# Performance work log

Measured on AMD Instinct MI355X. Metric: run time of the kernel, lower is better.

## Reference

```python
import jax, jax.numpy as jnp
import numpy as np

NUM_BINS = 16
TAU = 0.05
EPS_SUM = 1e-8
EPS_LOG = 1e-10


def _entropy(counts):
    # counts: (dim, bins) -> (dim,) entropy in bits
    probs = counts / jnp.clip(counts.sum(axis=-1, keepdims=True), EPS_SUM, None)
    return -(probs * jnp.log2(probs + EPS_LOG)).sum(axis=-1)


def setup_inputs() -> dict:
    key = jax.random.key(0)
    k1, k2 = jax.random.split(key)
    dim = 2097152
    observation = jax.random.normal(k1, (8, dim), dtype=jnp.float32)
    # positive histogram counts (buffer starts at ones in torch; randomize for a nontrivial test)
    belief_counts = jax.random.uniform(k2, (dim, NUM_BINS), dtype=jnp.float32)
    return {"observation": observation, "belief_counts": belief_counts}


def reference(observation, belief_counts):
    if observation.ndim == 2:
        observation = observation.mean(axis=0)  # (dim,)
    dim = observation.shape[0]

    prior_probs = belief_counts / jnp.clip(
        belief_counts.sum(axis=-1, keepdims=True), EPS_SUM, None)

    # sigmoid binning -> int bin indices in [0, NUM_BINS-1]
    normalized = jax.nn.sigmoid(observation)
    bins = jnp.clip((normalized * (NUM_BINS - 1)).astype(jnp.int32), 0, NUM_BINS - 1)

    one_hot = jax.nn.one_hot(bins, NUM_BINS, dtype=belief_counts.dtype)  # (dim, bins)
    posterior_counts = belief_counts + one_hot
    posterior_probs = posterior_counts / jnp.clip(
        posterior_counts.sum(axis=-1, keepdims=True), EPS_SUM, None)

    H_prior = _entropy(belief_counts)
    H_posterior = _entropy(posterior_counts)

    info_gain = jnp.clip(
        (posterior_probs * jnp.log2((posterior_probs + EPS_LOG) / (prior_probs + EPS_LOG))).sum(axis=-1),
        0.0, None)
    mean_info_gain = info_gain.mean()
    epistemic_value = jax.nn.sigmoid(mean_info_gain * 50.0 - 1.0)

    # EMA buffer update (no_grad in torch)
    new_belief_counts = jnp.clip(belief_counts * (1.0 - TAU) + one_hot * TAU, 0.01, None)

    return (info_gain, mean_info_gain, H_prior, H_posterior, epistemic_value,
            new_belief_counts)
```

## Files before the change

kernel.cpp:

```cpp
#include <hip/hip_runtime.h>
#include <math.h>

namespace {
constexpr float TAU      = 0.05f;
constexpr float EPS_SUM  = 1e-8f;
constexpr float EPS_LOG  = 1e-10f;
constexpr int   BLOCK    = 256;
constexpr int   GRID     = 2048;
}

__device__ inline float quad_sum(float x) {
    int a = __builtin_amdgcn_mov_dpp(__float_as_int(x), 0xB1, 0xF, 0xF, true);
    x += __int_as_float(a);
    a = __builtin_amdgcn_mov_dpp(__float_as_int(x), 0x4E, 0xF, 0xF, true);
    x += __int_as_float(a);
    return x;
}

__device__ inline float fast_log2(float x) { return __log2f(x); }
__device__ inline float fast_rcp(float x)  { return __builtin_amdgcn_rcpf(x); }

__device__ __forceinline__ float bin_from8(float o0, float o1, float o2, float o3,
                                           float o4, float o5, float o6, float o7) {
    float x0 = o0 + o1, x1 = o2 + o3, x2 = o4 + o5, x3 = o6 + o7;
    float os = (x0 + x1) + (x2 + x3);
    float om = os * 0.125f;
    float sig = 1.0f / (1.0f + expf(-om));
    int bin = (int)(sig * 15.0f);
    bin = bin < 0 ? 0 : (bin > 15 ? 15 : bin);
    return (float)bin;
}

__global__ __launch_bounds__(BLOCK) void ev_bins(
    const float* __restrict__ obs,
    float* __restrict__ bins,
    int dim)
{
    const int gid = blockIdx.x * BLOCK + threadIdx.x;
    const int gstride = BLOCK * gridDim.x;
    const int total4 = dim >> 2;
    const size_t d4 = (size_t)total4;
    const float4* obs4 = reinterpret_cast<const float4*>(obs);
    float4* bins4 = reinterpret_cast<float4*>(bins);

    for (int c = gid; c < total4; c += gstride) {
        float4 r0 = obs4[0 * d4 + c];
        float4 r1 = obs4[1 * d4 + c];
        float4 r2 = obs4[2 * d4 + c];
        float4 r3 = obs4[3 * d4 + c];
        float4 r4 = obs4[4 * d4 + c];
        float4 r5 = obs4[5 * d4 + c];
        float4 r6 = obs4[6 * d4 + c];
        float4 r7 = obs4[7 * d4 + c];
        float4 b;
        b.x = bin_from8(r0.x, r1.x, r2.x, r3.x, r4.x, r5.x, r6.x, r7.x);
        b.y = bin_from8(r0.y, r1.y, r2.y, r3.y, r4.y, r5.y, r6.y, r7.y);
        b.z = bin_from8(r0.z, r1.z, r2.z, r3.z, r4.z, r5.z, r6.z, r7.z);
        b.w = bin_from8(r0.w, r1.w, r2.w, r3.w, r4.w, r5.w, r6.w, r7.w);
        bins4[c] = b;
    }
    for (int c = total4 * 4 + gid; c < dim; c += gstride) {
        bins[c] = bin_from8(obs[0 * (size_t)dim + c], obs[1 * (size_t)dim + c],
                            obs[2 * (size_t)dim + c], obs[3 * (size_t)dim + c],
                            obs[4 * (size_t)dim + c], obs[5 * (size_t)dim + c],
                            obs[6 * (size_t)dim + c], obs[7 * (size_t)dim + c]);
    }
}

__device__ __forceinline__ void process_item(
    int f, float4 c4, int bin,
    float* __restrict__ out_info, float* __restrict__ out_Hprior,
    float* __restrict__ out_Hpost, float2* __restrict__ nb2,
    float& local_sum)
{
    const int r = f >> 2;
    const int m = f & 3;

    float cs = quad_sum((c4.x + c4.y) + (c4.z + c4.w));

    float inv_prior = fast_rcp(fmaxf(cs, EPS_SUM));
    float inv_post  = fast_rcp(fmaxf(cs + 1.0f, EPS_SUM));

    float Hpr = 0.0f, Hpo = 0.0f, ig = 0.0f;
    float cc[4] = {c4.x, c4.y, c4.z, c4.w};
    float nb[4];
    const int j0 = m * 4;
#pragma unroll
    for (int e = 0; e < 4; ++e) {
        float cj = cc[e];
        bool hit = (j0 + e == bin);
        float oh = hit ? 1.0f : 0.0f;
        float p  = cj * inv_prior;
        float pp = (cj + oh) * inv_post;
        float lp  = fast_log2(p  + EPS_LOG);
        float lpp = fast_log2(pp + EPS_LOG);
        Hpr -= p  * lp;
        Hpo -= pp * lpp;
        ig  += pp * (lpp - lp);
        nb[e] = fmaxf(fmaf(cj, 1.0f - TAU, hit ? TAU : 0.0f), 0.01f);
    }
    Hpr = quad_sum(Hpr);
    Hpo = quad_sum(Hpo);
    ig  = fmaxf(quad_sum(ig), 0.0f);
    local_sum += ig;

    if (m == 0) {
        out_info[r]   = ig;
        out_Hprior[r] = Hpr;
        out_Hpost[r]  = Hpo;
    }
    nb2[(size_t)f * 2]     = make_float2(nb[0], nb[1]);
    nb2[(size_t)f * 2 + 1] = make_float2(nb[2], nb[3]);
}

__global__ __launch_bounds__(BLOCK) void ev_main(
    const float* __restrict__ belief,
    const float* __restrict__ binsf,
    float* __restrict__ out_info,
    float* __restrict__ out_Hprior,
    float* __restrict__ out_Hpost,
    float* __restrict__ out_newbelief,
    float* __restrict__ ws_partials,
    int dim)
{
    const int tid    = blockIdx.x * BLOCK + threadIdx.x;
    const int stride = BLOCK * GRID;
    const int W      = dim * 4;
    const int step2  = 2 * stride;
    const int Wbulk  = W - (W % step2);
    float local_sum = 0.0f;

    const float4* belief4 = reinterpret_cast<const float4*>(belief);
    float2* nb2 = reinterpret_cast<float2*>(out_newbelief);

    int f = tid;
    float4 A0, A1;
    float b0, b1;
    if (f < Wbulk) {
        A0 = belief4[f];
        b0 = binsf[f >> 2];
        A1 = belief4[f + stride];
        b1 = binsf[(f + stride) >> 2];
    }

    for (; f < Wbulk; f += step2) {
        const int fp = f + step2;
        const bool more = (fp < Wbulk);
        const int g0 = more ? fp : f;
        const int g1 = more ? fp + stride : f;
        float4 P0 = belief4[g0];
        float  p0 = binsf[g0 >> 2];
        float4 P1 = belief4[g1];
        float  p1 = binsf[g1 >> 2];

        __builtin_amdgcn_sched_barrier(0);

        process_item(f,          A0, (int)b0,
                     out_info, out_Hprior, out_Hpost, nb2, local_sum);
        process_item(f + stride, A1, (int)b1,
                     out_info, out_Hprior, out_Hpost, nb2, local_sum);

        A0 = P0; b0 = p0;
        A1 = P1; b1 = p1;
    }

    for (; f < W; f += stride) {
        float4 c4 = belief4[f];
        int bin = (int)binsf[f >> 2];
        process_item(f, c4, bin,
                     out_info, out_Hprior, out_Hpost, nb2, local_sum);
    }

    __shared__ float sdata[BLOCK];
    sdata[threadIdx.x] = local_sum;
    __syncthreads();
#pragma unroll
    for (int off = BLOCK / 2; off > 0; off >>= 1) {
        if (threadIdx.x < off) sdata[threadIdx.x] += sdata[threadIdx.x + off];
        __syncthreads();
    }
    if (threadIdx.x == 0) ws_partials[blockIdx.x] = sdata[0];
}

__global__ __launch_bounds__(BLOCK) void ev_fused(
    const float* __restrict__ obs,
    const float* __restrict__ belief,
    float* __restrict__ out_info,
    float* __restrict__ out_Hprior,
    float* __restrict__ out_Hpost,
    float* __restrict__ out_newbelief,
    float* __restrict__ ws_partials,
    int dim)
{
    const int tid    = blockIdx.x * BLOCK + threadIdx.x;
    const int stride = BLOCK * GRID;
    const int W      = dim * 4;
    float local_sum = 0.0f;

    const float4* belief4 = reinterpret_cast<const float4*>(belief);
    float2* nb2 = reinterpret_cast<float2*>(out_newbelief);

    for (int f = tid; f < W; f += stride) {
        const int r = f >> 2;
        const int m = f & 3;
        float4 c4 = belief4[f];
        float oa = obs[(size_t)(2 * m) * dim + r];
        float ob = obs[(size_t)(2 * m + 1) * dim + r];
        float os = quad_sum(oa + ob);
        float om = os * 0.125f;
        float sig = 1.0f / (1.0f + expf(-om));
        int bin = (int)(sig * 15.0f);
        bin = bin < 0 ? 0 : (bin > 15 ? 15 : bin);
        process_item(f, c4, bin,
                     out_info, out_Hprior, out_Hpost, nb2, local_sum);
    }

    __shared__ float sdata[BLOCK];
    sdata[threadIdx.x] = local_sum;
    __syncthreads();
#pragma unroll
    for (int off = BLOCK / 2; off > 0; off >>= 1) {
        if (threadIdx.x < off) sdata[threadIdx.x] += sdata[threadIdx.x + off];
        __syncthreads();
    }
    if (threadIdx.x == 0) ws_partials[blockIdx.x] = sdata[0];
}

__global__ __launch_bounds__(BLOCK) void ev_finalize(
    const float* __restrict__ ws_partials,
    float* __restrict__ out_mean,
    float* __restrict__ out_epi,
    int n_partials, float inv_cnt)
{
    float s = 0.0f;
    for (int i = threadIdx.x; i < n_partials; i += BLOCK) s += ws_partials[i];
    __shared__ float sdata[BLOCK];
    sdata[threadIdx.x] = s;
    __syncthreads();
#pragma unroll
    for (int off = BLOCK / 2; off > 0; off >>= 1) {
        if (threadIdx.x < off) sdata[threadIdx.x] += sdata[threadIdx.x + off];
        __syncthreads();
    }
    if (threadIdx.x == 0) {
        float mean = sdata[0] * inv_cnt;
        *out_mean = mean;
        *out_epi  = 1.0f / (1.0f + expf(-(mean * 50.0f - 1.0f)));
    }
}

extern "C" void kernel_launch(void* const* d_in, const int* in_sizes, int n_in,
                              void* d_out, int out_size, void* d_ws, size_t ws_size,
                              hipStream_t stream)
{
    const float* obs    = (const float*)d_in[0];
    const float* belief = (const float*)d_in[1];
    const int dim = in_sizes[0] / 8;

    float* o             = (float*)d_out;
    float* out_info      = o;
    float* out_mean      = o + dim;
    float* out_Hprior    = o + dim + 1;
    float* out_Hpost     = o + 2 * (size_t)dim + 1;
    float* out_epi       = o + 3 * (size_t)dim + 1;
    float* out_newbelief = o + 3 * (size_t)dim + 2;

    float* partials = (float*)d_ws;
    float* bins     = (float*)d_ws + GRID;
    const size_t ws_needed = sizeof(float) * ((size_t)GRID + (size_t)dim);

    if (ws_size >= ws_needed) {
        ev_bins<<<GRID, BLOCK, 0, stream>>>(obs, bins, dim);
        ev_main<<<GRID, BLOCK, 0, stream>>>(belief, bins, out_info, out_Hprior,
                                            out_Hpost, out_newbelief, partials,
                                            dim);
    } else {
        ev_fused<<<GRID, BLOCK, 0, stream>>>(obs, belief, out_info, out_Hprior,
                                             out_Hpost, out_newbelief, partials,
                                             dim);
    }
    ev_finalize<<<1, BLOCK, 0, stream>>>(partials, out_mean, out_epi, GRID,
                                         1.0f / (4.0f * (float)dim));
}
```

Before: 313.2 us.

## Process one row per thread in main kernel instead of quad-lane rows

Rewrites the main kernel so each thread handles a full 16-bin row with four float4 loads, replacing the 4-lane-per-row scheme with DPP quad reductions and the double-buffered prefetch loop. This removes cross-lane shuffles and the reciprocal and reduction work each lane duplicated. Finalize scaling is adjusted because partial sums now hold one value per row. Per-instruction memory access becomes strided across lanes, and the explicit software prefetch is dropped.

```diff
diff --git a/kernel.cpp b/kernel.cpp
--- a/kernel.cpp
+++ b/kernel.cpp
@@ -67,7 +67,93 @@
     }
 }
 
-__device__ __forceinline__ void process_item(
+__global__ __launch_bounds__(BLOCK) void ev_main(
+    const float* __restrict__ belief,
+    const float* __restrict__ binsf,
+    float* __restrict__ out_info,
+    float* __restrict__ out_Hprior,
+    float* __restrict__ out_Hpost,
+    float* __restrict__ out_newbelief,
+    float* __restrict__ ws_partials,
+    int dim)
+{
+    const int tid    = blockIdx.x * BLOCK + threadIdx.x;
+    const int stride = BLOCK * GRID;
+    float local_sum = 0.0f;
+
+    const float4* belief4 = reinterpret_cast<const float4*>(belief);
+    float2* nb2 = reinterpret_cast<float2*>(out_newbelief);
+
+    for (int r = tid; r < dim; r += stride) {
+        const size_t r4 = (size_t)r * 4;
+        float4 c0 = belief4[r4 + 0];
+        float4 c1 = belief4[r4 + 1];
+        float4 c2 = belief4[r4 + 2];
+        float4 c3 = belief4[r4 + 3];
+        const int bin = (int)binsf[r];
+
+        float s0 = (c0.x + c0.y) + (c0.z + c0.w);
+        float s1 = (c1.x + c1.y) + (c1.z + c1.w);
+        float s2 = (c2.x + c2.y) + (c2.z + c2.w);
+        float s3 = (c3.x + c3.y) + (c3.z + c3.w);
+        float cs = (s0 + s1) + (s2 + s3);
+
+        float inv_prior = fast_rcp(fmaxf(cs, EPS_SUM));
+        float inv_post  = fast_rcp(fmaxf(cs + 1.0f, EPS_SUM));
+
+        float Hpr_g[4], Hpo_g[4], ig_g[4];
+        float2 nbo[8];
+        const float4 cg[4] = {c0, c1, c2, c3};
+#pragma unroll
+        for (int m = 0; m < 4; ++m) {
+            float cc[4] = {cg[m].x, cg[m].y, cg[m].z, cg[m].w};
+            float Hpr = 0.0f, Hpo = 0.0f, ig = 0.0f;
+            float nb[4];
+            const int j0 = m * 4;
+#pragma unroll
+            for (int e = 0; e < 4; ++e) {
+                float cj = cc[e];
+                bool hit = (j0 + e == bin);
+                float oh = hit ? 1.0f : 0.0f;
+                float p  = cj * inv_prior;
+                float pp = (cj + oh) * inv_post;
+                float lp  = fast_log2(p  + EPS_LOG);
+                float lpp = fast_log2(pp + EPS_LOG);
+                Hpr -= p  * lp;
+                Hpo -= pp * lpp;
+                ig  += pp * (lpp - lp);
+                nb[e] = fmaxf(fmaf(cj, 1.0f - TAU, hit ? TAU : 0.0f), 0.01f);
+            }
+            Hpr_g[m] = Hpr; Hpo_g[m] = Hpo; ig_g[m] = ig;
+            nbo[m * 2]     = make_float2(nb[0], nb[1]);
+            nbo[m * 2 + 1] = make_float2(nb[2], nb[3]);
+        }
+        float Hpr = (Hpr_g[0] + Hpr_g[1]) + (Hpr_g[2] + Hpr_g[3]);
+        float Hpo = (Hpo_g[0] + Hpo_g[1]) + (Hpo_g[2] + Hpo_g[3]);
+        float ig  = fmaxf((ig_g[0] + ig_g[1]) + (ig_g[2] + ig_g[3]), 0.0f);
+        local_sum += ig;
+
+        out_info[r]   = ig;
+        out_Hprior[r] = Hpr;
+        out_Hpost[r]  = Hpo;
+
+        const size_t nbase = (size_t)r * 8;
+#pragma unroll
+        for (int j = 0; j < 8; ++j) nb2[nbase + j] = nbo[j];
+    }
+
+    __shared__ float sdata[BLOCK];
+    sdata[threadIdx.x] = local_sum;
+    __syncthreads();
+#pragma unroll
+    for (int off = BLOCK / 2; off > 0; off >>= 1) {
+        if (threadIdx.x < off) sdata[threadIdx.x] += sdata[threadIdx.x + off];
+        __syncthreads();
+    }
+    if (threadIdx.x == 0) ws_partials[blockIdx.x] = sdata[0];
+}
+
+__device__ __forceinline__ void process_item_quad(
     int f, float4 c4, int bin,
     float* __restrict__ out_info, float* __restrict__ out_Hprior,
     float* __restrict__ out_Hpost, float2* __restrict__ nb2,
@@ -113,75 +199,6 @@
     nb2[(size_t)f * 2 + 1] = make_float2(nb[2], nb[3]);
 }
 
-__global__ __launch_bounds__(BLOCK) void ev_main(
-    const float* __restrict__ belief,
-    const float* __restrict__ binsf,
-    float* __restrict__ out_info,
-    float* __restrict__ out_Hprior,
-    float* __restrict__ out_Hpost,
-    float* __restrict__ out_newbelief,
-    float* __restrict__ ws_partials,
-    int dim)
-{
-    const int tid    = blockIdx.x * BLOCK + threadIdx.x;
-    const int stride = BLOCK * GRID;
-    const int W      = dim * 4;
-    const int step2  = 2 * stride;
-    const int Wbulk  = W - (W % step2);
-    float local_sum = 0.0f;
-
-    const float4* belief4 = reinterpret_cast<const float4*>(belief);
-    float2* nb2 = reinterpret_cast<float2*>(out_newbelief);
-
-    int f = tid;
-    float4 A0, A1;
-    float b0, b1;
-    if (f < Wbulk) {
-        A0 = belief4[f];
-        b0 = binsf[f >> 2];
-        A1 = belief4[f + stride];
-        b1 = binsf[(f + stride) >> 2];
-    }
-
-    for (; f < Wbulk; f += step2) {
-        const int fp = f + step2;
-        const bool more = (fp < Wbulk);
-        const int g0 = more ? fp : f;
-        const int g1 = more ? fp + stride : f;
-        float4 P0 = belief4[g0];
-        float  p0 = binsf[g0 >> 2];
-        float4 P1 = belief4[g1];
-        float  p1 = binsf[g1 >> 2];
-
-        __builtin_amdgcn_sched_barrier(0);
-
-        process_item(f,          A0, (int)b0,
-                     out_info, out_Hprior, out_Hpost, nb2, local_sum);
-        process_item(f + stride, A1, (int)b1,
-                     out_info, out_Hprior, out_Hpost, nb2, local_sum);
-
-        A0 = P0; b0 = p0;
-        A1 = P1; b1 = p1;
-    }
-
-    for (; f < W; f += stride) {
-        float4 c4 = belief4[f];
-        int bin = (int)binsf[f >> 2];
-        process_item(f, c4, bin,
-                     out_info, out_Hprior, out_Hpost, nb2, local_sum);
-    }
-
-    __shared__ float sdata[BLOCK];
-    sdata[threadIdx.x] = local_sum;
-    __syncthreads();
-#pragma unroll
-    for (int off = BLOCK / 2; off > 0; off >>= 1) {
-        if (threadIdx.x < off) sdata[threadIdx.x] += sdata[threadIdx.x + off];
-        __syncthreads();
-    }
-    if (threadIdx.x == 0) ws_partials[blockIdx.x] = sdata[0];
-}
-
 __global__ __launch_bounds__(BLOCK) void ev_fused(
     const float* __restrict__ obs,
     const float* __restrict__ belief,
@@ -211,8 +228,8 @@
         float sig = 1.0f / (1.0f + expf(-om));
         int bin = (int)(sig * 15.0f);
         bin = bin < 0 ? 0 : (bin > 15 ? 15 : bin);
-        process_item(f, c4, bin,
-                     out_info, out_Hprior, out_Hpost, nb2, local_sum);
+        process_item_quad(f, c4, bin,
+                          out_info, out_Hprior, out_Hpost, nb2, local_sum);
     }
 
     __shared__ float sdata[BLOCK];
@@ -274,11 +291,13 @@
         ev_main<<<GRID, BLOCK, 0, stream>>>(belief, bins, out_info, out_Hprior,
                                             out_Hpost, out_newbelief, partials,
                                             dim);
+        ev_finalize<<<1, BLOCK, 0, stream>>>(partials, out_mean, out_epi, GRID,
+                                             1.0f / (float)dim);
     } else {
         ev_fused<<<GRID, BLOCK, 0, stream>>>(obs, belief, out_info, out_Hprior,
                                              out_Hpost, out_newbelief, partials,
                                              dim);
-    }
-    ev_finalize<<<1, BLOCK, 0, stream>>>(partials, out_mean, out_epi, GRID,
-                                         1.0f / (4.0f * (float)dim));
-}
+        ev_finalize<<<1, BLOCK, 0, stream>>>(partials, out_mean, out_epi, GRID,
+                                             1.0f / (4.0f * (float)dim));
+    }
+}
```

Measured after the change: 322.3 us. +2.9%, slower.
